# Kernel optimization log

Hardware: AMD Instinct MI355X
Metric: run time of the kernel (lower is better)

## Reference

```python
import jax, jax.numpy as jnp
import numpy as np

TOP_K = 2  # num_experts_per_tok

def setup_inputs() -> dict:
    key = jax.random.key(0)
    ks = jax.random.split(key, 6)
    B, S, D, E, H = 4, 2048, 1024, 8, 4096
    x  = jax.random.normal(ks[0], (B, S, D), dtype=jnp.float32)
    Wg = jax.random.normal(ks[1], (D, E), dtype=jnp.float32) * 0.02
    W1 = jax.random.normal(ks[2], (E, D, H), dtype=jnp.float32) * 0.02
    b1 = jnp.zeros((E, H), dtype=jnp.float32)
    W2 = jax.random.normal(ks[3], (E, H, D), dtype=jnp.float32) * 0.02
    b2 = jnp.zeros((E, D), dtype=jnp.float32)
    return {"x": x, "Wg": Wg, "W1": W1, "b1": b1, "W2": W2, "b2": b2}

def reference(x, Wg, W1, b1, W2, b2):
    B, S, D = x.shape
    E = Wg.shape[1]
    xf = x.reshape(-1, D)                       # [T, D]
    T = xf.shape[0]
    logits = xf @ Wg                            # [T, E]
    probs = jax.nn.softmax(logits, axis=-1)
    weights, indices = jax.lax.top_k(probs, TOP_K)   # [T, K]
    # Dense combine weights: cw[t, e] = routing weight if e in top-k of t else 0.
    cw = jnp.zeros((T, E), dtype=x.dtype).at[jnp.arange(T)[:, None], indices].set(weights)
    out = jnp.zeros_like(xf)
    for e in range(E):  # small fixed expert count; per-expert GEMMs
        h = jax.nn.gelu(xf @ W1[e] + b1[e], approximate=False)  # [T, H]
        y = h @ W2[e] + b2[e]                                   # [T, D]
        out = out + y * cw[:, e:e + 1]
    return out.reshape(B, S, D)
```

## Files before the change

kernel.cpp:

```cpp
#include <hip/hip_runtime.h>
#include <hip/hip_bf16.h>
#include <stdint.h>

#define D_DIM 1024
#define E_NUM 8
#define H_DIM 4096

typedef __attribute__((ext_vector_type(8))) short short8;
typedef __attribute__((ext_vector_type(4))) short short4v;
typedef __attribute__((ext_vector_type(4))) unsigned short ushort4v;
typedef __attribute__((ext_vector_type(4))) float f32x4;

#define GLOBAL_AS __attribute__((address_space(1)))
#define LDS_AS __attribute__((address_space(3)))

__device__ __forceinline__ void async_load16(const void* g, void* l) {
    __builtin_amdgcn_global_load_lds((GLOBAL_AS void*)g, (LDS_AS void*)l, 16, 0, 0);
}

__device__ __forceinline__ float gelu_fast(float x) {
    float x3 = x * x * x;
    float z = 0.7978845608028654f * x + 0.0356774081363001f * x3;
    float u = __expf(-2.0f * fabsf(z));
    float t = __fdividef(1.0f - u, 1.0f + u);
    t = copysignf(t, z);
    return 0.5f * x * (1.0f + t);
}

__device__ __forceinline__ float b2f(short s) {
    union { float f; unsigned u; } x; x.u = ((unsigned)(unsigned short)s) << 16; return x.f;
}

__device__ __forceinline__ unsigned short f2b(float f) {
    union { __hip_bfloat16 h; unsigned short s; } u;
    u.h = __float2bfloat16(f);
    return u.s;
}

__global__ __launch_bounds__(256) void router_kernel(
    const float* __restrict__ x, const float* __restrict__ Wg,
    __hip_bfloat16* __restrict__ xb, int* __restrict__ epick,
    float* __restrict__ ewgt, int T) {
    int gwave = (int)((blockIdx.x * 256 + threadIdx.x) >> 6);
    int lane = threadIdx.x & 63;
    if (gwave >= T) return;
    const float* xr = x + (size_t)gwave * D_DIM;
    double acc[E_NUM];
#pragma unroll
    for (int e = 0; e < E_NUM; ++e) acc[e] = 0.0;
#pragma unroll
    for (int i = 0; i < D_DIM / 64; ++i) {
        int d = i * 64 + lane;
        float xv = xr[d];
        xb[(size_t)gwave * D_DIM + d] = __float2bfloat16(xv);
        const float4* wgp = (const float4*)(Wg + (size_t)d * E_NUM);
        float4 wa = wgp[0], wb = wgp[1];
        double xd = (double)xv;
        acc[0] += xd * (double)wa.x; acc[1] += xd * (double)wa.y;
        acc[2] += xd * (double)wa.z; acc[3] += xd * (double)wa.w;
        acc[4] += xd * (double)wb.x; acc[5] += xd * (double)wb.y;
        acc[6] += xd * (double)wb.z; acc[7] += xd * (double)wb.w;
    }
#pragma unroll
    for (int s = 32; s > 0; s >>= 1) {
#pragma unroll
        for (int e = 0; e < E_NUM; ++e) acc[e] += __shfl_xor(acc[e], s);
    }
    double mx = acc[0];
#pragma unroll
    for (int e = 1; e < E_NUM; ++e) mx = fmax(mx, acc[e]);
    double p[E_NUM]; double sum = 0.0;
#pragma unroll
    for (int e = 0; e < E_NUM; ++e) { p[e] = exp(acc[e] - mx); sum += p[e]; }
    int i0 = 0;
#pragma unroll
    for (int e = 1; e < E_NUM; ++e) if (p[e] > p[i0]) i0 = e;
    int i1 = (i0 == 0) ? 1 : 0;
#pragma unroll
    for (int e = 0; e < E_NUM; ++e) if (e != i0 && p[e] > p[i1]) i1 = e;
    if (lane == 0) {
        epick[gwave] = i0 | (i1 << 8);
        ewgt[2 * gwave]     = (float)(p[i0] / sum);
        ewgt[2 * gwave + 1] = (float)(p[i1] / sum);
    }
}

__global__ __launch_bounds__(256) void bucket_kernel(
    const int* __restrict__ epick, int* __restrict__ cnt,
    int* __restrict__ tok, int* __restrict__ eidx, int T) {
    __shared__ int lcnt[E_NUM];
    __shared__ int gbase[E_NUM];
    int b = blockIdx.x, tid = threadIdx.x;
    if (tid < E_NUM) lcnt[tid] = 0;
    __syncthreads();
    int t = b * 128 + (tid >> 1);
    int j = tid & 1;
    int e = (epick[t] >> (j * 8)) & 0xff;
    int li = atomicAdd(&lcnt[e], 1);
    __syncthreads();
    if (tid < E_NUM) gbase[tid] = atomicAdd(&cnt[tid], lcnt[tid]);
    __syncthreads();
    int slot = gbase[e] + li;
    tok[e * T + slot] = t;
    eidx[2 * t + j] = (e << 16) | slot;
}

__global__ void prefix_kernel(const int* __restrict__ cnt, int* __restrict__ base) {
    if (threadIdx.x == 0) {
        int a = 0;
#pragma unroll
        for (int e = 0; e < E_NUM; ++e) { base[e] = a; a += cnt[e]; }
    }
}

__global__ __launch_bounds__(256) void transpose_both_kernel(
    const float* __restrict__ W1, const float* __restrict__ W2,
    __hip_bfloat16* __restrict__ w1t, __hip_bfloat16* __restrict__ w2t) {
    __shared__ float tile[64][65];
    int e = blockIdx.z;
    int id = blockIdx.x;
    const float* src; unsigned short* dst; int R, C, r0, c0, perm;
    if (id < 1024) {
        R = D_DIM; C = H_DIM;
        r0 = (id >> 6) * 64; c0 = (id & 63) * 64;
        src = W1 + (size_t)e * D_DIM * H_DIM;
        dst = (unsigned short*)(w1t + (size_t)e * H_DIM * D_DIM);
        perm = 0;
    } else {
        id -= 1024;
        R = H_DIM; C = D_DIM;
        r0 = (id >> 4) * 64; c0 = (id & 15) * 64;
        src = W2 + (size_t)e * H_DIM * D_DIM;
        dst = (unsigned short*)(w2t + (size_t)e * D_DIM * H_DIM);
        perm = 1;
    }
    int tx = threadIdx.x, ty = threadIdx.y;
#pragma unroll
    for (int i = 0; i < 8; ++i) {
        int j = ty + i * 8;
        int sr = perm ? ((j & 3) * 16 + (j >> 2)) : j;
        float2 v = *(const float2*)(src + (size_t)(r0 + sr) * C + c0 + 2 * tx);
        tile[j][2 * tx] = v.x; tile[j][2 * tx + 1] = v.y;
    }
    __syncthreads();
#pragma unroll
    for (int i = 0; i < 8; ++i) {
        int cc = ty + i * 8;
        unsigned pk = (unsigned)f2b(tile[2 * tx][cc]) | ((unsigned)f2b(tile[2 * tx + 1][cc]) << 16);
        *(unsigned*)(dst + (size_t)(c0 + cc) * R + r0 + 2 * tx) = pk;
    }
}


__global__ __launch_bounds__(256) void gemm1_kernel(
    const __hip_bfloat16* __restrict__ xb,
    const __hip_bfloat16* __restrict__ w1t,
    const float* __restrict__ b1,
    const int* __restrict__ cnt, const int* __restrict__ base,
    const int* __restrict__ tok,
    __hip_bfloat16* __restrict__ hbuf,
    int T) {
    int e = blockIdx.z;
    int M = cnt[e];
    int m0 = blockIdx.y * 128;
    if (m0 >= M) return;
    int n0 = blockIdx.x * 128;
    const __hip_bfloat16* Bp = w1t + (size_t)e * H_DIM * D_DIM;

    __shared__ __align__(16) short sA[128 * 32];
    __shared__ __align__(16) short sB[128 * 32];
    __shared__ float sBias[128];
    char* sAc = (char*)sA; char* sBc = (char*)sB;

    int tid = threadIdx.x;
    int w = tid >> 6, lane = tid & 63;
    int wm = w >> 1, wn = w & 1;
    int q = lane >> 4, l4 = lane & 15;

    if (tid < 128) sBias[tid] = b1[e * H_DIM + n0 + tid];

    int kswz = ((lane & 3) ^ ((lane >> 3) & 3)) << 3;
    int r0 = w * 32 + (lane >> 2);
    int r1 = r0 + 16;
    int tA0 = tok[e * T + min(m0 + r0, M - 1)];
    int tA1 = tok[e * T + min(m0 + r1, M - 1)];
    const __hip_bfloat16* gA0 = xb + (size_t)tA0 * D_DIM + kswz;
    const __hip_bfloat16* gA1 = xb + (size_t)tA1 * D_DIM + kswz;
    const __hip_bfloat16* gB0 = Bp + (size_t)(n0 + r0) * D_DIM + kswz;
    const __hip_bfloat16* gB1 = Bp + (size_t)(n0 + r1) * D_DIM + kswz;
    char* lA0 = sAc + w * 2048 + (lane & 3) * 16 + (lane >> 2) * 64;
    char* lB0 = sBc + w * 2048 + (lane & 3) * 16 + (lane >> 2) * 64;
    lA0 = sAc + w * 2048 + lane * 16 - lane * 16 + lane * 16;
    lA0 = sAc + w * 2048 + lane * 16;
    lB0 = sBc + w * 2048 + lane * 16;
    char* lA1 = sAc + w * 2048 + 1024 + (lane * 16) - (lane * 16);
    lA1 = sAc + w * 2048 + 1024;
    char* lB1 = sBc + w * 2048 + 1024;
    lA1 += 0; lB1 += 0;

    f32x4 acc[4][4];
#pragma unroll
    for (int a = 0; a < 4; ++a)
#pragma unroll
        for (int b = 0; b < 4; ++b) acc[a][b] = (f32x4){0.f, 0.f, 0.f, 0.f};

    for (int kk = 0; kk < D_DIM; kk += 32) {
        async_load16(gA0 + kk, lA0);
        async_load16(gA1 + kk, lA1);
        async_load16(gB0 + kk, lB0);
        async_load16(gB1 + kk, lB1);
        __syncthreads();
        short8 aF[4], bF[4];
#pragma unroll
        for (int t = 0; t < 4; ++t) {
            int ra = wm * 64 + t * 16 + l4;
            aF[t] = *(const short8*)(sAc + ra * 64 + ((q ^ ((ra >> 1) & 3)) << 4));
            int rb = wn * 64 + t * 16 + l4;
            bF[t] = *(const short8*)(sBc + rb * 64 + ((q ^ ((rb >> 1) & 3)) << 4));
        }
#pragma unroll
        for (int tm = 0; tm < 4; ++tm)
#pragma unroll
            for (int tn = 0; tn < 4; ++tn)
                acc[tm][tn] = __builtin_amdgcn_mfma_f32_16x16x32_bf16(aF[tm], bF[tn], acc[tm][tn], 0, 0, 0);
        __syncthreads();
    }

    int sb = base[e];
    unsigned short* hs = (unsigned short*)hbuf;
#pragma unroll
    for (int tm = 0; tm < 4; ++tm) {
        int rbase = wm * 64 + tm * 16 + q * 4;
#pragma unroll
        for (int i = 0; i < 4; ++i) {
            int row = m0 + rbase + i;
            if (row < M) {
                size_t hrow = (size_t)(sb + row) * H_DIM;
                ushort4v pk;
#pragma unroll
                for (int tn = 0; tn < 4; ++tn) {
                    float v = acc[tm][tn][i] + sBias[wn * 64 + tn * 16 + l4];
                    pk[tn] = f2b(gelu_fast(v));
                }
                *(ushort4v*)(hs + hrow + n0 + wn * 64 + l4 * 4) = pk;
            }
        }
    }
}

__global__ __launch_bounds__(256) void gemm2_kernel(
    const __hip_bfloat16* __restrict__ hbuf,
    const __hip_bfloat16* __restrict__ w2t,
    const int* __restrict__ cnt, const int* __restrict__ base,
    __hip_bfloat16* __restrict__ ybuf,
    int T) {
    int e = blockIdx.z >> 1;
    int kc = blockIdx.z & 1;
    int M = cnt[e];
    int m0 = blockIdx.y * 128;
    if (m0 >= M) return;
    int n0 = blockIdx.x * 128;
    int sb = base[e];
    const __hip_bfloat16* Bp = w2t + (size_t)e * D_DIM * H_DIM;

    __shared__ __align__(16) short sA[128 * 32];
    __shared__ __align__(16) short sB[128 * 32];
    char* sAc = (char*)sA; char* sBc = (char*)sB;

    int tid = threadIdx.x;
    int w = tid >> 6, lane = tid & 63;
    int wm = w >> 1, wn = w & 1;
    int q = lane >> 4, l4 = lane & 15;

    int kswz = ((lane & 3) ^ ((lane >> 3) & 3)) << 3;
    int r0 = w * 32 + (lane >> 2);
    int r1 = r0 + 16;
    const __hip_bfloat16* gA0 = hbuf + (size_t)(sb + min(m0 + r0, M - 1)) * H_DIM + kswz;
    const __hip_bfloat16* gA1 = hbuf + (size_t)(sb + min(m0 + r1, M - 1)) * H_DIM + kswz;
    const __hip_bfloat16* gB0 = Bp + (size_t)(n0 + r0) * H_DIM + kswz;
    const __hip_bfloat16* gB1 = Bp + (size_t)(n0 + r1) * H_DIM + kswz;
    char* lA0 = sAc + w * 2048 + lane * 16;
    char* lB0 = sBc + w * 2048 + lane * 16;
    char* lA1 = sAc + w * 2048 + 1024;
    char* lB1 = sBc + w * 2048 + 1024;

    f32x4 acc[4][4];
#pragma unroll
    for (int a = 0; a < 4; ++a)
#pragma unroll
        for (int b = 0; b < 4; ++b) acc[a][b] = (f32x4){0.f, 0.f, 0.f, 0.f};

    int k0 = kc * (H_DIM / 2), k1 = k0 + (H_DIM / 2);
    for (int kk = k0; kk < k1; kk += 32) {
        async_load16(gA0 + kk, lA0);
        async_load16(gA1 + kk, lA1);
        async_load16(gB0 + kk, lB0);
        async_load16(gB1 + kk, lB1);
        __syncthreads();
        short8 aF[4], bF[4];
#pragma unroll
        for (int t = 0; t < 4; ++t) {
            int ra = wm * 64 + t * 16 + l4;
            aF[t] = *(const short8*)(sAc + ra * 64 + ((q ^ ((ra >> 1) & 3)) << 4));
            int rb = wn * 64 + t * 16 + l4;
            bF[t] = *(const short8*)(sBc + rb * 64 + ((q ^ ((rb >> 1) & 3)) << 4));
        }
#pragma unroll
        for (int tm = 0; tm < 4; ++tm)
#pragma unroll
            for (int tn = 0; tn < 4; ++tn)
                acc[tm][tn] = __builtin_amdgcn_mfma_f32_16x16x32_bf16(aF[tm], bF[tn], acc[tm][tn], 0, 0, 0);
        __syncthreads();
    }

    size_t ybase = (size_t)kc * 2 * T;
    unsigned short* ys = (unsigned short*)ybuf;
#pragma unroll
    for (int tm = 0; tm < 4; ++tm) {
        int rbase = wm * 64 + tm * 16 + q * 4;
#pragma unroll
        for (int i = 0; i < 4; ++i) {
            int row = m0 + rbase + i;
            if (row < M) {
                size_t yrow = (ybase + sb + row) * D_DIM;
                ushort4v pk;
#pragma unroll
                for (int tn = 0; tn < 4; ++tn) pk[tn] = f2b(acc[tm][tn][i]);
                *(ushort4v*)(ys + yrow + n0 + wn * 64 + l4 * 4) = pk;
            }
        }
    }
}

__global__ __launch_bounds__(256) void combine_kernel(
    const __hip_bfloat16* __restrict__ yb, const float* __restrict__ b2,
    const int* __restrict__ base, const int* __restrict__ eidx,
    const float* __restrict__ ewgt, float* __restrict__ out, int T) {
    int t = blockIdx.x, tid = threadIdx.x;
    int v0 = eidx[2 * t], v1 = eidx[2 * t + 1];
    float w0 = ewgt[2 * t], w1 = ewgt[2 * t + 1];
    int e0 = v0 >> 16, e1 = v1 >> 16;
    size_t g0 = (size_t)base[e0] + (v0 & 0xffff);
    size_t g1 = (size_t)base[e1] + (v1 & 0xffff);
    int c = tid * 4;
    int blk = c >> 6;
    int tt = (c >> 2) & 15;
    size_t off2 = (size_t)2 * T * D_DIM;
    const short* ys = (const short*)yb;
    short4v a0 = *(const short4v*)(ys + g0 * D_DIM + c);
    short4v a1 = *(const short4v*)(ys + off2 + g0 * D_DIM + c);
    short4v c0 = *(const short4v*)(ys + g1 * D_DIM + c);
    short4v c1 = *(const short4v*)(ys + off2 + g1 * D_DIM + c);
    float s0[4] = { b2f(a0.x) + b2f(a1.x), b2f(a0.y) + b2f(a1.y),
                    b2f(a0.z) + b2f(a1.z), b2f(a0.w) + b2f(a1.w) };
    float s1[4] = { b2f(c0.x) + b2f(c1.x), b2f(c0.y) + b2f(c1.y),
                    b2f(c0.z) + b2f(c1.z), b2f(c0.w) + b2f(c1.w) };
    float* orow = out + (size_t)t * D_DIM;
#pragma unroll
    for (int s = 0; s < 4; ++s) {
        int oc = blk * 64 + s * 16 + tt;
        float o = w0 * (s0[s] + b2[(size_t)e0 * D_DIM + oc]) +
                  w1 * (s1[s] + b2[(size_t)e1 * D_DIM + oc]);
        orow[oc] = o;
    }
}

extern "C" void kernel_launch(void* const* d_in, const int* in_sizes, int n_in,
                              void* d_out, int out_size, void* d_ws, size_t ws_size,
                              hipStream_t stream) {
    const float* x  = (const float*)d_in[0];
    const float* Wg = (const float*)d_in[1];
    const float* W1 = (const float*)d_in[2];
    const float* b1 = (const float*)d_in[3];
    const float* W2 = (const float*)d_in[4];
    const float* b2 = (const float*)d_in[5];
    int T = in_sizes[0] / D_DIM;

    char* p = (char*)d_ws;
    int* cnt   = (int*)p;
    int* base  = (int*)(p + 256);
    int* tok   = (int*)(p + 512);
    int* eidx  = (int*)(p + 512 + 4ll * E_NUM * T);
    float* ewgt = (float*)(p + 512 + 4ll * E_NUM * T + 8ll * T);
    int* epick = (int*)(p + 512 + 4ll * E_NUM * T + 16ll * T);
    char* pb = p + 512 + 4ll * E_NUM * T + 20ll * T;
    __hip_bfloat16* xb  = (__hip_bfloat16*)pb;
    __hip_bfloat16* w1t = xb + (size_t)T * D_DIM;
    __hip_bfloat16* w2t = w1t + (size_t)E_NUM * H_DIM * D_DIM;
    __hip_bfloat16* hb  = w2t + (size_t)E_NUM * H_DIM * D_DIM;
    __hip_bfloat16* yb  = xb;

    hipMemsetAsync(cnt, 0, 256, stream);

    router_kernel<<<dim3((T + 3) / 4), 256, 0, stream>>>(x, Wg, xb, epick, ewgt, T);
    bucket_kernel<<<dim3(T / 128), 256, 0, stream>>>(epick, cnt, tok, eidx, T);
    prefix_kernel<<<1, 64, 0, stream>>>(cnt, base);
    transpose_both_kernel<<<dim3(2048, 1, E_NUM), dim3(32, 8), 0, stream>>>(W1, W2, w1t, w2t);
    gemm1_kernel<<<dim3(H_DIM / 128, T / 128, E_NUM), 256, 0, stream>>>(xb, w1t, b1, cnt, base, tok, hb, T);
    gemm2_kernel<<<dim3(D_DIM / 128, T / 128, E_NUM * 2), 256, 0, stream>>>(hb, w2t, cnt, base, yb, T);
    combine_kernel<<<T, 256, 0, stream>>>(yb, b2, base, eidx, ewgt, (float*)d_out, T);
}
```

Baseline: 737.2 us.

## Use 256x256 tiles with a 4-stage async LDS pipeline in expert GEMMs

Both expert GEMM kernels move from 128x128 tiles with 4 waves to 256x256 tiles with 8 waves, each wave now computing a 128x64 sub-tile. A 4-deep ring of LDS buffers is filled by async global-to-LDS loads issued three k-steps ahead. Explicit vmcnt waits and one barrier per step replace the two syncthreads per iteration, and MFMA sections are bracketed with s_setprio. The aim is to hide memory latency and raise data reuse per tile. In exchange it uses about 128KB of LDS and more accumulator registers, which limits occupancy, and it gives coarser work granularity for experts that receive few tokens.

```diff
diff --git a/kernel.cpp b/kernel.cpp
--- a/kernel.cpp
+++ b/kernel.cpp
@@ -152,7 +152,7 @@
 }
 
 
-__global__ __launch_bounds__(256) void gemm1_kernel(
+__global__ __launch_bounds__(512) void gemm1_kernel(
     const __hip_bfloat16* __restrict__ xb,
     const __hip_bfloat16* __restrict__ w1t,
     const float* __restrict__ b1,
@@ -162,22 +162,21 @@
     int T) {
     int e = blockIdx.z;
     int M = cnt[e];
-    int m0 = blockIdx.y * 128;
+    int m0 = blockIdx.y * 256;
     if (m0 >= M) return;
-    int n0 = blockIdx.x * 128;
+    int n0 = blockIdx.x * 256;
     const __hip_bfloat16* Bp = w1t + (size_t)e * H_DIM * D_DIM;
 
-    __shared__ __align__(16) short sA[128 * 32];
-    __shared__ __align__(16) short sB[128 * 32];
-    __shared__ float sBias[128];
-    char* sAc = (char*)sA; char* sBc = (char*)sB;
+    __shared__ __align__(16) short sA[4][256 * 32];
+    __shared__ __align__(16) short sB[4][256 * 32];
+    __shared__ float sBias[256];
 
     int tid = threadIdx.x;
     int w = tid >> 6, lane = tid & 63;
-    int wm = w >> 1, wn = w & 1;
+    int wm = w >> 2, wn = w & 3;
     int q = lane >> 4, l4 = lane & 15;
 
-    if (tid < 128) sBias[tid] = b1[e * H_DIM + n0 + tid];
+    if (tid < 256) sBias[tid] = b1[e * H_DIM + n0 + tid];
 
     int kswz = ((lane & 3) ^ ((lane >> 3) & 3)) << 3;
     int r0 = w * 32 + (lane >> 2);
@@ -188,49 +187,67 @@
     const __hip_bfloat16* gA1 = xb + (size_t)tA1 * D_DIM + kswz;
     const __hip_bfloat16* gB0 = Bp + (size_t)(n0 + r0) * D_DIM + kswz;
     const __hip_bfloat16* gB1 = Bp + (size_t)(n0 + r1) * D_DIM + kswz;
-    char* lA0 = sAc + w * 2048 + (lane & 3) * 16 + (lane >> 2) * 64;
-    char* lB0 = sBc + w * 2048 + (lane & 3) * 16 + (lane >> 2) * 64;
-    lA0 = sAc + w * 2048 + lane * 16 - lane * 16 + lane * 16;
-    lA0 = sAc + w * 2048 + lane * 16;
-    lB0 = sBc + w * 2048 + lane * 16;
-    char* lA1 = sAc + w * 2048 + 1024 + (lane * 16) - (lane * 16);
-    lA1 = sAc + w * 2048 + 1024;
-    char* lB1 = sBc + w * 2048 + 1024;
-    lA1 += 0; lB1 += 0;
-
-    f32x4 acc[4][4];
-#pragma unroll
-    for (int a = 0; a < 4; ++a)
+
+    f32x4 acc[8][4];
+#pragma unroll
+    for (int a = 0; a < 8; ++a)
 #pragma unroll
         for (int b = 0; b < 4; ++b) acc[a][b] = (f32x4){0.f, 0.f, 0.f, 0.f};
 
-    for (int kk = 0; kk < D_DIM; kk += 32) {
-        async_load16(gA0 + kk, lA0);
-        async_load16(gA1 + kk, lA1);
-        async_load16(gB0 + kk, lB0);
-        async_load16(gB1 + kk, lB1);
-        __syncthreads();
-        short8 aF[4], bF[4];
-#pragma unroll
-        for (int t = 0; t < 4; ++t) {
-            int ra = wm * 64 + t * 16 + l4;
-            aF[t] = *(const short8*)(sAc + ra * 64 + ((q ^ ((ra >> 1) & 3)) << 4));
-            int rb = wn * 64 + t * 16 + l4;
-            bF[t] = *(const short8*)(sBc + rb * 64 + ((q ^ ((rb >> 1) & 3)) << 4));
-        }
-#pragma unroll
-        for (int tm = 0; tm < 4; ++tm)
-#pragma unroll
-            for (int tn = 0; tn < 4; ++tn)
-                acc[tm][tn] = __builtin_amdgcn_mfma_f32_16x16x32_bf16(aF[tm], bF[tn], acc[tm][tn], 0, 0, 0);
-        __syncthreads();
-    }
+    auto stage = [&](int tt) {
+        int bi = tt & 3, kk = tt * 32;
+        char* la = (char*)sA[bi] + w * 2048;
+        char* lb = (char*)sB[bi] + w * 2048;
+        async_load16(gA0 + kk, la);
+        async_load16(gA1 + kk, la + 1024);
+        async_load16(gB0 + kk, lb);
+        async_load16(gB1 + kk, lb + 1024);
+    };
+    auto body = [&](int tt) {
+        const char* pa = (const char*)sA[tt & 3];
+        const char* pb = (const char*)sB[tt & 3];
+        short8 bF[4];
+#pragma unroll
+        for (int n = 0; n < 4; ++n) {
+            int rb = wn * 64 + n * 16 + l4;
+            bF[n] = *(const short8*)(pb + rb * 64 + ((q ^ ((rb >> 1) & 3)) << 4));
+        }
+        __builtin_amdgcn_s_setprio(1);
+#pragma unroll
+        for (int m = 0; m < 8; ++m) {
+            int ra = wm * 128 + m * 16 + l4;
+            short8 aF = *(const short8*)(pa + ra * 64 + ((q ^ ((ra >> 1) & 3)) << 4));
+#pragma unroll
+            for (int n = 0; n < 4; ++n)
+                acc[m][n] = __builtin_amdgcn_mfma_f32_16x16x32_bf16(aF, bF[n], acc[m][n], 0, 0, 0);
+        }
+        __builtin_amdgcn_s_setprio(0);
+    };
+
+    const int nt = D_DIM / 32;
+    asm volatile("s_waitcnt vmcnt(0)" ::: "memory");
+    stage(0); stage(1); stage(2);
+    asm volatile("s_waitcnt vmcnt(8)" ::: "memory");
+    __builtin_amdgcn_s_barrier();
+    for (int t = 0; t < nt - 3; ++t) {
+        stage(t + 3);
+        body(t);
+        asm volatile("s_waitcnt vmcnt(8)" ::: "memory");
+        __builtin_amdgcn_s_barrier();
+    }
+    body(nt - 3);
+    asm volatile("s_waitcnt vmcnt(4)" ::: "memory");
+    __builtin_amdgcn_s_barrier();
+    body(nt - 2);
+    asm volatile("s_waitcnt vmcnt(0)" ::: "memory");
+    __builtin_amdgcn_s_barrier();
+    body(nt - 1);
 
     int sb = base[e];
     unsigned short* hs = (unsigned short*)hbuf;
 #pragma unroll
-    for (int tm = 0; tm < 4; ++tm) {
-        int rbase = wm * 64 + tm * 16 + q * 4;
+    for (int m = 0; m < 8; ++m) {
+        int rbase = wm * 128 + m * 16 + q * 4;
 #pragma unroll
         for (int i = 0; i < 4; ++i) {
             int row = m0 + rbase + i;
@@ -238,9 +255,9 @@
                 size_t hrow = (size_t)(sb + row) * H_DIM;
                 ushort4v pk;
 #pragma unroll
-                for (int tn = 0; tn < 4; ++tn) {
-                    float v = acc[tm][tn][i] + sBias[wn * 64 + tn * 16 + l4];
-                    pk[tn] = f2b(gelu_fast(v));
+                for (int n = 0; n < 4; ++n) {
+                    float v = acc[m][n][i] + sBias[wn * 64 + n * 16 + l4];
+                    pk[n] = f2b(gelu_fast(v));
                 }
                 *(ushort4v*)(hs + hrow + n0 + wn * 64 + l4 * 4) = pk;
             }
@@ -248,7 +265,7 @@
     }
 }
 
-__global__ __launch_bounds__(256) void gemm2_kernel(
+__global__ __launch_bounds__(512) void gemm2_kernel(
     const __hip_bfloat16* __restrict__ hbuf,
     const __hip_bfloat16* __restrict__ w2t,
     const int* __restrict__ cnt, const int* __restrict__ base,
@@ -257,67 +274,89 @@
     int e = blockIdx.z >> 1;
     int kc = blockIdx.z & 1;
     int M = cnt[e];
-    int m0 = blockIdx.y * 128;
+    int m0 = blockIdx.y * 256;
     if (m0 >= M) return;
-    int n0 = blockIdx.x * 128;
+    int n0 = blockIdx.x * 256;
     int sb = base[e];
     const __hip_bfloat16* Bp = w2t + (size_t)e * D_DIM * H_DIM;
 
-    __shared__ __align__(16) short sA[128 * 32];
-    __shared__ __align__(16) short sB[128 * 32];
-    char* sAc = (char*)sA; char* sBc = (char*)sB;
+    __shared__ __align__(16) short sA[4][256 * 32];
+    __shared__ __align__(16) short sB[4][256 * 32];
 
     int tid = threadIdx.x;
     int w = tid >> 6, lane = tid & 63;
-    int wm = w >> 1, wn = w & 1;
+    int wm = w >> 2, wn = w & 3;
     int q = lane >> 4, l4 = lane & 15;
 
     int kswz = ((lane & 3) ^ ((lane >> 3) & 3)) << 3;
     int r0 = w * 32 + (lane >> 2);
     int r1 = r0 + 16;
-    const __hip_bfloat16* gA0 = hbuf + (size_t)(sb + min(m0 + r0, M - 1)) * H_DIM + kswz;
-    const __hip_bfloat16* gA1 = hbuf + (size_t)(sb + min(m0 + r1, M - 1)) * H_DIM + kswz;
-    const __hip_bfloat16* gB0 = Bp + (size_t)(n0 + r0) * H_DIM + kswz;
-    const __hip_bfloat16* gB1 = Bp + (size_t)(n0 + r1) * H_DIM + kswz;
-    char* lA0 = sAc + w * 2048 + lane * 16;
-    char* lB0 = sBc + w * 2048 + lane * 16;
-    char* lA1 = sAc + w * 2048 + 1024;
-    char* lB1 = sBc + w * 2048 + 1024;
-
-    f32x4 acc[4][4];
-#pragma unroll
-    for (int a = 0; a < 4; ++a)
+    int k0 = kc * (H_DIM / 2);
+    const __hip_bfloat16* gA0 = hbuf + (size_t)(sb + min(m0 + r0, M - 1)) * H_DIM + k0 + kswz;
+    const __hip_bfloat16* gA1 = hbuf + (size_t)(sb + min(m0 + r1, M - 1)) * H_DIM + k0 + kswz;
+    const __hip_bfloat16* gB0 = Bp + (size_t)(n0 + r0) * H_DIM + k0 + kswz;
+    const __hip_bfloat16* gB1 = Bp + (size_t)(n0 + r1) * H_DIM + k0 + kswz;
+
+    f32x4 acc[8][4];
+#pragma unroll
+    for (int a = 0; a < 8; ++a)
 #pragma unroll
         for (int b = 0; b < 4; ++b) acc[a][b] = (f32x4){0.f, 0.f, 0.f, 0.f};
 
-    int k0 = kc * (H_DIM / 2), k1 = k0 + (H_DIM / 2);
-    for (int kk = k0; kk < k1; kk += 32) {
-        async_load16(gA0 + kk, lA0);
-        async_load16(gA1 + kk, lA1);
-        async_load16(gB0 + kk, lB0);
-        async_load16(gB1 + kk, lB1);
-        __syncthreads();
-        short8 aF[4], bF[4];
-#pragma unroll
-        for (int t = 0; t < 4; ++t) {
-            int ra = wm * 64 + t * 16 + l4;
-            aF[t] = *(const short8*)(sAc + ra * 64 + ((q ^ ((ra >> 1) & 3)) << 4));
-            int rb = wn * 64 + t * 16 + l4;
-            bF[t] = *(const short8*)(sBc + rb * 64 + ((q ^ ((rb >> 1) & 3)) << 4));
-        }
-#pragma unroll
-        for (int tm = 0; tm < 4; ++tm)
-#pragma unroll
-            for (int tn = 0; tn < 4; ++tn)
-                acc[tm][tn] = __builtin_amdgcn_mfma_f32_16x16x32_bf16(aF[tm], bF[tn], acc[tm][tn], 0, 0, 0);
-        __syncthreads();
-    }
+    auto stage = [&](int tt) {
+        int bi = tt & 3, kk = tt * 32;
+        char* la = (char*)sA[bi] + w * 2048;
+        char* lb = (char*)sB[bi] + w * 2048;
+        async_load16(gA0 + kk, la);
+        async_load16(gA1 + kk, la + 1024);
+        async_load16(gB0 + kk, lb);
+        async_load16(gB1 + kk, lb + 1024);
+    };
+    auto body = [&](int tt) {
+        const char* pa = (const char*)sA[tt & 3];
+        const char* pb = (const char*)sB[tt & 3];
+        short8 bF[4];
+#pragma unroll
+        for (int n = 0; n < 4; ++n) {
+            int rb = wn * 64 + n * 16 + l4;
+            bF[n] = *(const short8*)(pb + rb * 64 + ((q ^ ((rb >> 1) & 3)) << 4));
+        }
+        __builtin_amdgcn_s_setprio(1);
+#pragma unroll
+        for (int m = 0; m < 8; ++m) {
+            int ra = wm * 128 + m * 16 + l4;
+            short8 aF = *(const short8*)(pa + ra * 64 + ((q ^ ((ra >> 1) & 3)) << 4));
+#pragma unroll
+            for (int n = 0; n < 4; ++n)
+                acc[m][n] = __builtin_amdgcn_mfma_f32_16x16x32_bf16(aF, bF[n], acc[m][n], 0, 0, 0);
+        }
+        __builtin_amdgcn_s_setprio(0);
+    };
+
+    const int nt = (H_DIM / 2) / 32;
+    asm volatile("s_waitcnt vmcnt(0)" ::: "memory");
+    stage(0); stage(1); stage(2);
+    asm volatile("s_waitcnt vmcnt(8)" ::: "memory");
+    __builtin_amdgcn_s_barrier();
+    for (int t = 0; t < nt - 3; ++t) {
+        stage(t + 3);
+        body(t);
+        asm volatile("s_waitcnt vmcnt(8)" ::: "memory");
+        __builtin_amdgcn_s_barrier();
+    }
+    body(nt - 3);
+    asm volatile("s_waitcnt vmcnt(4)" ::: "memory");
+    __builtin_amdgcn_s_barrier();
+    body(nt - 2);
+    asm volatile("s_waitcnt vmcnt(0)" ::: "memory");
+    __builtin_amdgcn_s_barrier();
+    body(nt - 1);
 
     size_t ybase = (size_t)kc * 2 * T;
     unsigned short* ys = (unsigned short*)ybuf;
 #pragma unroll
-    for (int tm = 0; tm < 4; ++tm) {
-        int rbase = wm * 64 + tm * 16 + q * 4;
+    for (int m = 0; m < 8; ++m) {
+        int rbase = wm * 128 + m * 16 + q * 4;
 #pragma unroll
         for (int i = 0; i < 4; ++i) {
             int row = m0 + rbase + i;
@@ -325,7 +364,7 @@
                 size_t yrow = (ybase + sb + row) * D_DIM;
                 ushort4v pk;
 #pragma unroll
-                for (int tn = 0; tn < 4; ++tn) pk[tn] = f2b(acc[tm][tn][i]);
+                for (int n = 0; n < 4; ++n) pk[n] = f2b(acc[m][n][i]);
                 *(ushort4v*)(ys + yrow + n0 + wn * 64 + l4 * 4) = pk;
             }
         }
@@ -396,7 +435,7 @@
     bucket_kernel<<<dim3(T / 128), 256, 0, stream>>>(epick, cnt, tok, eidx, T);
     prefix_kernel<<<1, 64, 0, stream>>>(cnt, base);
     transpose_both_kernel<<<dim3(2048, 1, E_NUM), dim3(32, 8), 0, stream>>>(W1, W2, w1t, w2t);
-    gemm1_kernel<<<dim3(H_DIM / 128, T / 128, E_NUM), 256, 0, stream>>>(xb, w1t, b1, cnt, base, tok, hb, T);
-    gemm2_kernel<<<dim3(D_DIM / 128, T / 128, E_NUM * 2), 256, 0, stream>>>(hb, w2t, cnt, base, yb, T);
+    gemm1_kernel<<<dim3(H_DIM / 256, T / 256, E_NUM), 512, 0, stream>>>(xb, w1t, b1, cnt, base, tok, hb, T);
+    gemm2_kernel<<<dim3(D_DIM / 256, T / 256, E_NUM * 2), 512, 0, stream>>>(hb, w2t, cnt, base, yb, T);
     combine_kernel<<<T, 256, 0, stream>>>(yb, b2, base, eidx, ewgt, (float*)d_out, T);
 }
```

Result: slower. 882.2 us (+19.7%).
